# Kernel optimization log

Measured on AMD Instinct MI355X. Metric: run time of the kernel, lower is better.

## Reference

```python
import jax, jax.numpy as jnp
import numpy as np

H = 1024          # hidden_dim; also the attention 'sequence' length (embed_dim=1)
L = 12            # n_layers per stack (att1 and att2 each have L blocks)
FF = 4 * H        # MLP expansion
B, CT_DIM, CL_DIM = 8, 2048, 128
EPS = 1e-5


def _ln(x, g, b):
    m = jnp.mean(x, axis=-1, keepdims=True)
    v = jnp.mean((x - m) ** 2, axis=-1, keepdims=True)
    return (x - m) / jnp.sqrt(v + EPS) * g + b


def setup_inputs() -> dict:
    key = jax.random.key(0)
    ks = jax.random.split(key, 8)

    def w(k, shape, s=0.02):
        return (jax.random.normal(k, shape) * s).astype(jnp.float32)

    inp = {
        "ct": jax.random.normal(ks[0], (B, CT_DIM), jnp.float32),
        "clinical": jax.random.normal(ks[1], (B, CL_DIM), jnp.float32),
        "W_ct": w(ks[2], (CT_DIM, H)), "b_ct": jnp.zeros((H,), jnp.float32),
        "W_cl": w(ks[3], (CL_DIM, H)), "b_cl": jnp.zeros((H,), jnp.float32),
        "norm_g": jnp.ones((2 * H,), jnp.float32),
        "norm_b": jnp.zeros((2 * H,), jnp.float32),
    }
    for i, pre in enumerate(("att1", "att2")):
        kk = jax.random.split(ks[4 + i], 4)
        inp[pre + "_inw"] = w(kk[0], (L, 3), 0.5)      # q,k,v scalar in-proj weights (embed_dim=1)
        inp[pre + "_inb"] = jnp.zeros((L, 3), jnp.float32)
        inp[pre + "_ow"] = w(kk[1], (L,), 0.5)          # scalar out-proj weight
        inp[pre + "_ob"] = jnp.zeros((L,), jnp.float32)
        inp[pre + "_g1"] = jnp.ones((L, H), jnp.float32)
        inp[pre + "_be1"] = jnp.zeros((L, H), jnp.float32)
        inp[pre + "_g2"] = jnp.ones((L, H), jnp.float32)
        inp[pre + "_be2"] = jnp.zeros((L, H), jnp.float32)
        inp[pre + "_W1"] = w(kk[2], (L, H, FF))
        inp[pre + "_b1"] = jnp.zeros((L, FF), jnp.float32)
        inp[pre + "_W2"] = w(kk[3], (L, FF, H))
        inp[pre + "_b2"] = jnp.zeros((L, H), jnp.float32)
    return inp


def _stack(query, kv, params):
    # query is fixed across the stack; kv is the carried state (matches
    # Scale_Dot_Attention returning (query, kv, kv) through nn.Sequential).
    def step(kv, p):
        inw, inb, ow, ob, g1, be1, g2, be2, W1, b1, W2, b2 = p
        v = _ln(kv, g1, be1)                              # norm1(value)  [B,H]
        # embed_dim=1 MHA: scalar in-projections, scale = 1/sqrt(1) = 1
        qp = query * inw[0] + inb[0]                      # [B,H]
        kp = kv * inw[1] + inb[1]                         # [B,H]
        vp = v * inw[2] + inb[2]                          # [B,H]
        attn = jax.nn.softmax(qp[:, :, None] * kp[:, None, :], axis=-1)  # [B,H,H]
        av = jnp.einsum('bqk,bk->bq', attn, vp) * ow + ob                # out-proj
        out = _ln(av + v, g2, be2)                        # norm2(attn + normed value)
        out = out + jax.nn.gelu(out @ W1 + b1, approximate=False) @ W2 + b2
        return out, None
    kv, _ = jax.lax.scan(step, kv, params)
    return kv


def _forward(ct, clinical, W_ct, b_ct, W_cl, b_cl,
             att1_inw, att1_inb, att1_ow, att1_ob, att1_g1, att1_be1,
             att1_g2, att1_be2, att1_W1, att1_b1, att1_W2, att1_b2,
             att2_inw, att2_inb, att2_ow, att2_ob, att2_g1, att2_be1,
             att2_g2, att2_be2, att2_W1, att2_b1, att2_W2, att2_b2,
             norm_g, norm_b):
    cte = ct @ W_ct + b_ct            # [B,H]
    cle = clinical @ W_cl + b_cl      # [B,H]
    p1 = (att1_inw, att1_inb, att1_ow, att1_ob, att1_g1, att1_be1,
          att1_g2, att1_be2, att1_W1, att1_b1, att1_W2, att1_b2)
    p2 = (att2_inw, att2_inb, att2_ow, att2_ob, att2_g1, att2_be1,
          att2_g2, att2_be2, att2_W1, att2_b1, att2_W2, att2_b2)
    ct_attn = _stack(cle, cte, p1)    # att1: query=clinical, kv=ct
    cl_attn = _stack(cte, cle, p2)    # att2: query=ct, kv=clinical
    return _ln(jnp.concatenate([ct_attn, cl_attn], axis=1), norm_g, norm_b)


def reference(ct, clinical, W_ct, b_ct, W_cl, b_cl,
              att1_inw, att1_inb, att1_ow, att1_ob, att1_g1, att1_be1,
              att1_g2, att1_be2, att1_W1, att1_b1, att1_W2, att1_b2,
              att2_inw, att2_inb, att2_ow, att2_ob, att2_g1, att2_be1,
              att2_g2, att2_be2, att2_W1, att2_b1, att2_W2, att2_b2,
              norm_g, norm_b):
    return _forward(ct, clinical, W_ct, b_ct, W_cl, b_cl,
                    att1_inw, att1_inb, att1_ow, att1_ob, att1_g1, att1_be1,
                    att1_g2, att1_be2, att1_W1, att1_b1, att1_W2, att1_b2,
                    att2_inw, att2_inb, att2_ow, att2_ob, att2_g1, att2_be1,
                    att2_g2, att2_be2, att2_W1, att2_b1, att2_W2, att2_b2,
                    norm_g, norm_b)
```

## Files before the change

kernel.cpp:

```cpp
#include <hip/hip_runtime.h>
#include <cstddef>

namespace {

constexpr int kH = 1024;
constexpr int kFF = 4096;
constexpr int kB = 8;
constexpr int kL = 12;
constexpr float kEps = 1e-5f;

struct StackParams {
  const float *inw, *inb, *ow, *ob, *g1, *be1, *g2, *be2, *W1, *b1, *W2, *b2;
};

__device__ __forceinline__ void blkReduceSum2(float& a, float& c, float* red) {
#pragma unroll
  for (int m = 1; m < 64; m <<= 1) { a += __shfl_xor(a, m); c += __shfl_xor(c, m); }
  int w = threadIdx.x >> 6;
  __syncthreads();
  if ((threadIdx.x & 63) == 0) { red[w] = a; red[4 + w] = c; }
  __syncthreads();
  a = red[0] + red[1] + red[2] + red[3];
  c = red[4] + red[5] + red[6] + red[7];
}

__device__ __forceinline__ void blkReduceMaxMin(float& a, float& c, float* red) {
#pragma unroll
  for (int m = 1; m < 64; m <<= 1) {
    a = fmaxf(a, __shfl_xor(a, m));
    c = fminf(c, __shfl_xor(c, m));
  }
  int w = threadIdx.x >> 6;
  __syncthreads();
  if ((threadIdx.x & 63) == 0) { red[w] = a; red[4 + w] = c; }
  __syncthreads();
  a = fmaxf(fmaxf(red[0], red[1]), fmaxf(red[2], red[3]));
  c = fminf(fminf(red[4], red[5]), fminf(red[6], red[7]));
}

template <int KC>
__global__ __launch_bounds__(256) void gemvPart(const float* __restrict__ X,
                                                const float* __restrict__ W,
                                                float* __restrict__ part,
                                                int K, int N) {
  const int FT = N >> 10;
  int ft = blockIdx.x % FT;
  int kc = blockIdx.x / FT;
  int k0 = kc * KC;
  __shared__ float Xs[kB][KC];
  int t = threadIdx.x;
  for (int i = t; i < kB * KC; i += 256) {
    int b = i / KC, kk = i % KC;
    Xs[b][kk] = X[(size_t)b * K + k0 + kk];
  }
  __syncthreads();
  int c0 = (ft << 10) + (t << 2);
  float acc[kB][4];
#pragma unroll
  for (int b = 0; b < kB; ++b)
#pragma unroll
    for (int j = 0; j < 4; ++j) acc[b][j] = 0.f;
  const float* Wp = W + (size_t)k0 * N + c0;
#pragma unroll
  for (int kk = 0; kk < KC; ++kk) {
    float4 w = *reinterpret_cast<const float4*>(Wp + (size_t)kk * N);
#pragma unroll
    for (int b = 0; b < kB; ++b) {
      float x = Xs[b][kk];
      acc[b][0] = fmaf(x, w.x, acc[b][0]);
      acc[b][1] = fmaf(x, w.y, acc[b][1]);
      acc[b][2] = fmaf(x, w.z, acc[b][2]);
      acc[b][3] = fmaf(x, w.w, acc[b][3]);
    }
  }
  float* pp = part + (size_t)kc * kB * N + c0;
#pragma unroll
  for (int b = 0; b < kB; ++b) {
    *reinterpret_cast<float4*>(pp + (size_t)b * N) =
        make_float4(acc[b][0], acc[b][1], acc[b][2], acc[b][3]);
  }
}

__global__ __launch_bounds__(256) void embedReduce(const float* __restrict__ pct,
                                                   const float* __restrict__ pcl,
                                                   const float* __restrict__ b_ct,
                                                   const float* __restrict__ b_cl,
                                                   float* __restrict__ emb,
                                                   float* __restrict__ kv) {
  int id = blockIdx.x * 256 + threadIdx.x;
  int s = id >> 13;
  int bn = id & 8191;
  int n = id & 1023;
  float sum;
  if (s == 0) {
    sum = b_ct[n];
#pragma unroll 4
    for (int p = 0; p < 128; ++p) sum += pct[(size_t)p * 8192 + bn];
  } else {
    sum = b_cl[n];
#pragma unroll 4
    for (int p = 0; p < 32; ++p) sum += pcl[(size_t)p * 8192 + bn];
  }
  emb[id] = sum;
  kv[id] = sum;
}

__global__ __launch_bounds__(256) void attnKernel(const float* __restrict__ kv,
                                                  const float* __restrict__ emb,
                                                  float* __restrict__ y2,
                                                  StackParams P0, StackParams P1,
                                                  int l) {
  int bid = blockIdx.x;
  int s = bid >> 8;
  int b = (bid >> 5) & 7;
  int qt = bid & 31;
  StackParams P = s ? P1 : P0;
  const float* kvr = kv + ((size_t)((s << 3) + b)) * kH;
  const float* qr = emb + ((size_t)(((1 - s) << 3) + b)) * kH;
  float wi0 = P.inw[l * 3 + 0], wi1 = P.inw[l * 3 + 1], wi2 = P.inw[l * 3 + 2];
  float bi0 = P.inb[l * 3 + 0], bi1 = P.inb[l * 3 + 1], bi2 = P.inb[l * 3 + 2];
  float ow = P.ow[l], ob = P.ob[l];
  const float* g1 = P.g1 + (size_t)l * kH;
  const float* be1 = P.be1 + (size_t)l * kH;

  __shared__ float kvs[kH];
  __shared__ float2 kvp[kH];
  __shared__ float red[8];

  int t = threadIdx.x;
  float lsum = 0.f, lsq = 0.f;
#pragma unroll
  for (int i = 0; i < 4; ++i) {
    float x = kvr[t + 256 * i];
    kvs[t + 256 * i] = x;
    lsum += x;
    lsq += x * x;
  }
  blkReduceSum2(lsum, lsq, red);
  float mean = lsum * (1.f / kH);
  float rstd = rsqrtf(lsq * (1.f / kH) - mean * mean + kEps);

  float lmax = -1e30f, lmin = 1e30f;
#pragma unroll
  for (int i = 0; i < 4; ++i) {
    int k = t + 256 * i;
    float x = kvs[k];
    float kp = fmaf(x, wi1, bi1);
    float v = (x - mean) * rstd * g1[k] + be1[k];
    float vp = fmaf(v, wi2, bi2);
    kvp[k] = make_float2(kp, vp);
    lmax = fmaxf(lmax, kp);
    lmin = fminf(lmin, kp);
  }
  blkReduceMaxMin(lmax, lmin, red);
  __syncthreads();

  int q = (qt << 5) + (t >> 3);
  int ks = t & 7;
  float sq = fmaf(qr[q], wi0, bi0);
  float mb = fmaxf(sq * lmax, sq * lmin);
  float den0 = 0.f, num0 = 0.f, den1 = 0.f, num1 = 0.f;
#pragma unroll 4
  for (int j = 0; j < 128; j += 2) {
    float2 a = kvp[ks + (j << 3)];
    float2 c = kvp[ks + ((j + 1) << 3)];
    float e0 = __expf(fmaf(sq, a.x, -mb));
    float e1 = __expf(fmaf(sq, c.x, -mb));
    den0 += e0; num0 = fmaf(e0, a.y, num0);
    den1 += e1; num1 = fmaf(e1, c.y, num1);
  }
  float den = den0 + den1, num = num0 + num1;
#pragma unroll
  for (int m = 1; m < 8; m <<= 1) {
    den += __shfl_xor(den, m);
    num += __shfl_xor(num, m);
  }
  if (ks == 0) {
    float av = num / den;
    float vq = (kvs[q] - mean) * rstd * g1[q] + be1[q];
    y2[((size_t)((s << 3) + b)) * kH + q] = fmaf(av, ow, ob) + vq;
  }
}

__global__ __launch_bounds__(256) void gemm1Kernel(const float* __restrict__ y2,
                                                   float* __restrict__ xn,
                                                   float* __restrict__ part1,
                                                   StackParams P0, StackParams P1,
                                                   int l) {
  int bid = blockIdx.x;
  int s = bid >> 8;
  int ft = (bid >> 6) & 3;
  int kc = bid & 63;
  StackParams P = s ? P1 : P0;
  const float* y2s = y2 + ((size_t)s << 13);
  __shared__ float sm[kB], sr[kB];
  __shared__ float Xs[kB][16];
  int t = threadIdx.x;
  {
    int b = t >> 5, lane = t & 31;
    const float* row = y2s + (size_t)b * kH;
    float sum = 0.f, sq = 0.f;
    for (int i = lane; i < kH; i += 32) {
      float x = row[i];
      sum += x;
      sq += x * x;
    }
#pragma unroll
    for (int m = 1; m < 32; m <<= 1) { sum += __shfl_xor(sum, m); sq += __shfl_xor(sq, m); }
    if (lane == 0) {
      float mean = sum * (1.f / kH);
      sm[b] = mean;
      sr[b] = rsqrtf(sq * (1.f / kH) - mean * mean + kEps);
    }
  }
  __syncthreads();
  int k0 = kc << 4;
  if (t < 128) {
    int b = t >> 4, kk = t & 15, k = k0 + kk;
    float x = y2s[(size_t)b * kH + k];
    float v = (x - sm[b]) * sr[b] * P.g2[(size_t)l * kH + k] + P.be2[(size_t)l * kH + k];
    Xs[b][kk] = v;
    if (ft == 0) xn[((size_t)s << 13) + (size_t)b * kH + k] = v;
  }
  __syncthreads();
  int c0 = (ft << 10) + (t << 2);
  const float* W = P.W1 + (size_t)l * kH * kFF + (size_t)k0 * kFF + c0;
  float acc[kB][4];
#pragma unroll
  for (int b = 0; b < kB; ++b)
#pragma unroll
    for (int j = 0; j < 4; ++j) acc[b][j] = 0.f;
#pragma unroll
  for (int kk = 0; kk < 16; ++kk) {
    float4 w = *reinterpret_cast<const float4*>(W + (size_t)kk * kFF);
#pragma unroll
    for (int b = 0; b < kB; ++b) {
      float x = Xs[b][kk];
      acc[b][0] = fmaf(x, w.x, acc[b][0]);
      acc[b][1] = fmaf(x, w.y, acc[b][1]);
      acc[b][2] = fmaf(x, w.z, acc[b][2]);
      acc[b][3] = fmaf(x, w.w, acc[b][3]);
    }
  }
  float* pp = part1 + ((size_t)(s * 64 + kc) * kB) * kFF + c0;
#pragma unroll
  for (int b = 0; b < kB; ++b) {
    *reinterpret_cast<float4*>(pp + (size_t)b * kFF) =
        make_float4(acc[b][0], acc[b][1], acc[b][2], acc[b][3]);
  }
}

__global__ __launch_bounds__(256) void gemm2Kernel(const float* __restrict__ part1,
                                                   float* __restrict__ part2,
                                                   StackParams P0, StackParams P1,
                                                   int l) {
  int bid = blockIdx.x;
  int s = bid >> 8;
  int kc = bid & 255;
  StackParams P = s ? P1 : P0;
  int k0 = kc << 4;
  __shared__ float Xs[kB][16];
  int t = threadIdx.x;
  if (t < 128) {
    int b = t >> 4, kk = t & 15;
    const float* pp = part1 + (size_t)s * 64 * kB * kFF + (size_t)b * kFF + k0 + kk;
    float sum = P.b1[(size_t)l * kFF + k0 + kk];
#pragma unroll 8
    for (int p = 0; p < 64; ++p) sum += pp[(size_t)p * kB * kFF];
    Xs[b][kk] = 0.5f * sum * (1.f + erff(sum * 0.70710678118654752f));
  }
  __syncthreads();
  int c0 = t << 2;
  const float* W = P.W2 + (size_t)l * kFF * kH + (size_t)k0 * kH + c0;
  float acc[kB][4];
#pragma unroll
  for (int b = 0; b < kB; ++b)
#pragma unroll
    for (int j = 0; j < 4; ++j) acc[b][j] = 0.f;
#pragma unroll
  for (int kk = 0; kk < 16; ++kk) {
    float4 w = *reinterpret_cast<const float4*>(W + (size_t)kk * kH);
#pragma unroll
    for (int b = 0; b < kB; ++b) {
      float x = Xs[b][kk];
      acc[b][0] = fmaf(x, w.x, acc[b][0]);
      acc[b][1] = fmaf(x, w.y, acc[b][1]);
      acc[b][2] = fmaf(x, w.z, acc[b][2]);
      acc[b][3] = fmaf(x, w.w, acc[b][3]);
    }
  }
  float* pp = part2 + ((size_t)(s * 256 + kc) * kB) * kH + c0;
#pragma unroll
  for (int b = 0; b < kB; ++b) {
    *reinterpret_cast<float4*>(pp + (size_t)b * kH) =
        make_float4(acc[b][0], acc[b][1], acc[b][2], acc[b][3]);
  }
}

__global__ __launch_bounds__(256) void reduce2Kernel(const float* __restrict__ part2,
                                                     const float* __restrict__ xn,
                                                     float* __restrict__ kv,
                                                     StackParams P0, StackParams P1,
                                                     int l) {
  int gid = blockIdx.x * 256 + threadIdx.x;
  int o = gid >> 2;
  int ks = gid & 3;
  int s = o >> 13;
  int bn = o & 8191;
  int n = o & 1023;
  const float* pp = part2 + (size_t)s * 256 * 8192 + (size_t)ks * 8192 + bn;
  float sum = 0.f;
#pragma unroll 8
  for (int j = 0; j < 64; ++j) sum += pp[(size_t)j * 4 * 8192];
  sum += __shfl_xor(sum, 1);
  sum += __shfl_xor(sum, 2);
  if (ks == 0) {
    StackParams P = s ? P1 : P0;
    kv[o] = sum + P.b2[(size_t)l * kH + n] + xn[o];
  }
}

__global__ __launch_bounds__(256) void finalLn(const float* __restrict__ kv,
                                               const float* __restrict__ g,
                                               const float* __restrict__ bb,
                                               float* __restrict__ out) {
  int b = blockIdx.x;
  int t = threadIdx.x;
  __shared__ float red[8];
  float vals[8];
  float sum = 0.f, sq = 0.f;
#pragma unroll
  for (int i = 0; i < 8; ++i) {
    int idx = t + 256 * i;
    int s = idx >> 10, n = idx & 1023;
    float x = kv[(size_t)s * 8192 + (size_t)b * kH + n];
    vals[i] = x;
    sum += x;
    sq += x * x;
  }
  blkReduceSum2(sum, sq, red);
  float mean = sum * (1.f / 2048.f);
  float rstd = rsqrtf(sq * (1.f / 2048.f) - mean * mean + kEps);
#pragma unroll
  for (int i = 0; i < 8; ++i) {
    int idx = t + 256 * i;
    out[(size_t)b * 2048 + idx] = (vals[i] - mean) * rstd * g[idx] + bb[idx];
  }
}

}

extern "C" void kernel_launch(void* const* d_in, const int* in_sizes, int n_in,
                              void* d_out, int out_size, void* d_ws, size_t ws_size,
                              hipStream_t stream) {
  const float* ct = (const float*)d_in[0];
  const float* clinical = (const float*)d_in[1];
  const float* W_ct = (const float*)d_in[2];
  const float* b_ct = (const float*)d_in[3];
  const float* W_cl = (const float*)d_in[4];
  const float* b_cl = (const float*)d_in[5];
  const float* norm_g = (const float*)d_in[6];
  const float* norm_b = (const float*)d_in[7];

  StackParams P0{(const float*)d_in[8],  (const float*)d_in[9],  (const float*)d_in[10],
                 (const float*)d_in[11], (const float*)d_in[12], (const float*)d_in[13],
                 (const float*)d_in[14], (const float*)d_in[15], (const float*)d_in[16],
                 (const float*)d_in[17], (const float*)d_in[18], (const float*)d_in[19]};
  StackParams P1{(const float*)d_in[20], (const float*)d_in[21], (const float*)d_in[22],
                 (const float*)d_in[23], (const float*)d_in[24], (const float*)d_in[25],
                 (const float*)d_in[26], (const float*)d_in[27], (const float*)d_in[28],
                 (const float*)d_in[29], (const float*)d_in[30], (const float*)d_in[31]};

  float* ws = (float*)d_ws;
  float* emb = ws;
  float* kv = emb + 2 * kB * kH;
  float* y2 = kv + 2 * kB * kH;
  float* xn = y2 + 2 * kB * kH;
  float* part1 = xn + 2 * kB * kH;
  float* part2 = part1 + (size_t)2 * 64 * kB * kFF;
  float* pct = part1;
  float* pcl = part1 + (size_t)128 * kB * kH;

  gemvPart<16><<<128, 256, 0, stream>>>(ct, W_ct, pct, 2048, 1024);
  gemvPart<4><<<32, 256, 0, stream>>>(clinical, W_cl, pcl, 128, 1024);
  embedReduce<<<64, 256, 0, stream>>>(pct, pcl, b_ct, b_cl, emb, kv);

  for (int l = 0; l < kL; ++l) {
    attnKernel<<<512, 256, 0, stream>>>(kv, emb, y2, P0, P1, l);
    gemm1Kernel<<<512, 256, 0, stream>>>(y2, xn, part1, P0, P1, l);
    gemm2Kernel<<<512, 256, 0, stream>>>(part1, part2, P0, P1, l);
    reduce2Kernel<<<256, 256, 0, stream>>>(part2, xn, kv, P0, P1, l);
  }

  finalLn<<<8, 256, 0, stream>>>(kv, norm_g, norm_b, (float*)d_out);
}
```

Measured before the change: 627.8 us.

## Fuse whole forward into one persistent cooperative kernel with grid syncs

```diff
diff --git a/kernel.cpp b/kernel.cpp
--- a/kernel.cpp
+++ b/kernel.cpp
@@ -1,5 +1,8 @@
 #include <hip/hip_runtime.h>
+#include <hip/hip_cooperative_groups.h>
 #include <cstddef>
+
+namespace cg = cooperative_groups;
 
 namespace {
 
@@ -8,23 +11,33 @@
 constexpr int kB = 8;
 constexpr int kL = 12;
 constexpr float kEps = 1e-5f;
+constexpr int NBLK = 256;
+constexpr int NTHR = 512;
 
 struct StackParams {
   const float *inw, *inb, *ow, *ob, *g1, *be1, *g2, *be2, *W1, *b1, *W2, *b2;
 };
 
-__device__ __forceinline__ void blkReduceSum2(float& a, float& c, float* red) {
+struct KArgs {
+  float *emb, *kv0, *y2, *xn, *part1, *part2, *pct, *pcl;
+  const float *ct, *clinical, *W_ct, *b_ct, *W_cl, *b_cl, *norm_g, *norm_b;
+  StackParams P0, P1;
+  float* out;
+};
+
+__device__ __forceinline__ void blkRed2(float& a, float& c, float* red) {
 #pragma unroll
   for (int m = 1; m < 64; m <<= 1) { a += __shfl_xor(a, m); c += __shfl_xor(c, m); }
   int w = threadIdx.x >> 6;
   __syncthreads();
-  if ((threadIdx.x & 63) == 0) { red[w] = a; red[4 + w] = c; }
-  __syncthreads();
-  a = red[0] + red[1] + red[2] + red[3];
-  c = red[4] + red[5] + red[6] + red[7];
-}
-
-__device__ __forceinline__ void blkReduceMaxMin(float& a, float& c, float* red) {
+  if ((threadIdx.x & 63) == 0) { red[w] = a; red[8 + w] = c; }
+  __syncthreads();
+  a = 0.f; c = 0.f;
+#pragma unroll
+  for (int j = 0; j < 8; ++j) { a += red[j]; c += red[8 + j]; }
+}
+
+__device__ __forceinline__ void blkRedMaxMin(float& a, float& c, float* red) {
 #pragma unroll
   for (int m = 1; m < 64; m <<= 1) {
     a = fmaxf(a, __shfl_xor(a, m));
@@ -32,319 +45,278 @@
   }
   int w = threadIdx.x >> 6;
   __syncthreads();
-  if ((threadIdx.x & 63) == 0) { red[w] = a; red[4 + w] = c; }
-  __syncthreads();
-  a = fmaxf(fmaxf(red[0], red[1]), fmaxf(red[2], red[3]));
-  c = fminf(fminf(red[4], red[5]), fminf(red[6], red[7]));
-}
-
-template <int KC>
-__global__ __launch_bounds__(256) void gemvPart(const float* __restrict__ X,
-                                                const float* __restrict__ W,
-                                                float* __restrict__ part,
-                                                int K, int N) {
-  const int FT = N >> 10;
-  int ft = blockIdx.x % FT;
-  int kc = blockIdx.x / FT;
-  int k0 = kc * KC;
-  __shared__ float Xs[kB][KC];
-  int t = threadIdx.x;
-  for (int i = t; i < kB * KC; i += 256) {
-    int b = i / KC, kk = i % KC;
-    Xs[b][kk] = X[(size_t)b * K + k0 + kk];
-  }
-  __syncthreads();
-  int c0 = (ft << 10) + (t << 2);
+  if ((threadIdx.x & 63) == 0) { red[w] = a; red[8 + w] = c; }
+  __syncthreads();
+  float ra = red[0], rc = red[8];
+#pragma unroll
+  for (int j = 1; j < 8; ++j) { ra = fmaxf(ra, red[j]); rc = fminf(rc, red[8 + j]); }
+  a = ra; c = rc;
+}
+
+__device__ __forceinline__ void reduce8store(float acc[kB][4], float* s_red,
+                                             float* dst, int N, int c0, int t) {
+  int w = t >> 6, lane = t & 63;
+  float* slot = s_red + (size_t)((w & 3) * 64 + lane) * 33;
+  if (w >= 4) {
+#pragma unroll
+    for (int f = 0; f < 32; ++f) slot[f] = acc[f >> 2][f & 3];
+  }
+  __syncthreads();
+  if (w < 4) {
+#pragma unroll
+    for (int f = 0; f < 32; ++f) slot[f] += acc[f >> 2][f & 3];
+  }
+  __syncthreads();
+  if (t < 256) {
+    int lane2 = t & 63, p = t >> 6;
+#pragma unroll
+    for (int bb = 0; bb < 2; ++bb) {
+      int b = p * 2 + bb, f0 = b * 4;
+      float4 s = make_float4(0.f, 0.f, 0.f, 0.f);
+#pragma unroll
+      for (int ww = 0; ww < 4; ++ww) {
+        const float* q = s_red + (size_t)(ww * 64 + lane2) * 33 + f0;
+        s.x += q[0]; s.y += q[1]; s.z += q[2]; s.w += q[3];
+      }
+      *reinterpret_cast<float4*>(dst + (size_t)b * N + c0 + lane2 * 4) = s;
+    }
+  }
+  __syncthreads();
+}
+
+template <int RPW, int ROWS>
+__device__ __forceinline__ void gemvTile(const float* __restrict__ Wrow, int N,
+                                         const float* Xs, float* dstSlice,
+                                         int c0, float* s_red, int t) {
+  int w = t >> 6, lane = t & 63;
   float acc[kB][4];
 #pragma unroll
-  for (int b = 0; b < kB; ++b)
-#pragma unroll
-    for (int j = 0; j < 4; ++j) acc[b][j] = 0.f;
-  const float* Wp = W + (size_t)k0 * N + c0;
-#pragma unroll
-  for (int kk = 0; kk < KC; ++kk) {
-    float4 w = *reinterpret_cast<const float4*>(Wp + (size_t)kk * N);
+  for (int b = 0; b < kB; ++b) { acc[b][0] = acc[b][1] = acc[b][2] = acc[b][3] = 0.f; }
+  const float* Wp = Wrow + (size_t)(w * RPW) * N + c0 + (lane << 2);
+#pragma unroll
+  for (int i = 0; i < RPW; ++i) {
+    float4 wv = *reinterpret_cast<const float4*>(Wp + (size_t)i * N);
+    int r = w * RPW + i;
 #pragma unroll
     for (int b = 0; b < kB; ++b) {
-      float x = Xs[b][kk];
-      acc[b][0] = fmaf(x, w.x, acc[b][0]);
-      acc[b][1] = fmaf(x, w.y, acc[b][1]);
-      acc[b][2] = fmaf(x, w.z, acc[b][2]);
-      acc[b][3] = fmaf(x, w.w, acc[b][3]);
-    }
-  }
-  float* pp = part + (size_t)kc * kB * N + c0;
-#pragma unroll
-  for (int b = 0; b < kB; ++b) {
-    *reinterpret_cast<float4*>(pp + (size_t)b * N) =
-        make_float4(acc[b][0], acc[b][1], acc[b][2], acc[b][3]);
-  }
-}
-
-__global__ __launch_bounds__(256) void embedReduce(const float* __restrict__ pct,
-                                                   const float* __restrict__ pcl,
-                                                   const float* __restrict__ b_ct,
-                                                   const float* __restrict__ b_cl,
-                                                   float* __restrict__ emb,
-                                                   float* __restrict__ kv) {
-  int id = blockIdx.x * 256 + threadIdx.x;
-  int s = id >> 13;
-  int bn = id & 8191;
-  int n = id & 1023;
-  float sum;
-  if (s == 0) {
-    sum = b_ct[n];
+      float x = Xs[b * ROWS + r];
+      acc[b][0] = fmaf(x, wv.x, acc[b][0]);
+      acc[b][1] = fmaf(x, wv.y, acc[b][1]);
+      acc[b][2] = fmaf(x, wv.z, acc[b][2]);
+      acc[b][3] = fmaf(x, wv.w, acc[b][3]);
+    }
+  }
+  reduce8store(acc, s_red, dstSlice, N, c0, t);
+}
+
+__global__ __launch_bounds__(NTHR, 2) void fusedAll(KArgs a) {
+  cg::grid_group grid = cg::this_grid();
+  __shared__ float s_xs[1024];
+  __shared__ float s_red[4 * 64 * 33];
+  __shared__ float s_stats[32];
+
+  const int bid = blockIdx.x;
+  const int t = threadIdx.x;
+
+  if (bid < 128) {
+    int kc = bid >> 2, fc = bid & 3;
+    int k0 = kc * 64, c0 = fc * 256;
+    { int b = t >> 6, r = t & 63; s_xs[b * 64 + r] = a.ct[b * 2048 + k0 + r]; }
+    __syncthreads();
+    gemvTile<8, 64>(a.W_ct + (size_t)k0 * kH, kH, s_xs,
+                    a.pct + (size_t)kc * kB * kH, c0, s_red, t);
+  } else if (bid < 160) {
+    int bb = bid - 128;
+    int kc = bb >> 2, fc = bb & 3;
+    int k0 = kc * 16, c0 = fc * 256;
+    if (t < 128) { int b = t >> 4, r = t & 15; s_xs[b * 16 + r] = a.clinical[b * 128 + k0 + r]; }
+    __syncthreads();
+    gemvTile<2, 16>(a.W_cl + (size_t)k0 * kH, kH, s_xs,
+                    a.pcl + (size_t)kc * kB * kH, c0, s_red, t);
+  }
+  grid.sync();
+
+  if (bid < 32) {
+    int id = bid * NTHR + t;
+    int s = id >> 13, n = id & 1023, bn = id & 8191;
+    float sum;
+    if (s == 0) {
+      sum = a.b_ct[n];
+      const float* pp = a.pct + bn;
 #pragma unroll 4
-    for (int p = 0; p < 128; ++p) sum += pct[(size_t)p * 8192 + bn];
-  } else {
-    sum = b_cl[n];
+      for (int p = 0; p < 32; ++p) sum += pp[(size_t)p * 8192];
+    } else {
+      sum = a.b_cl[n];
+      const float* pp = a.pcl + bn;
+#pragma unroll
+      for (int p = 0; p < 8; ++p) sum += pp[(size_t)p * 8192];
+    }
+    a.emb[id] = sum;
+    a.kv0[id] = sum;
+  }
+  grid.sync();
+
+  for (int l = 0; l < kL; ++l) {
+    {
+      int s = bid >> 7, b = (bid >> 4) & 7, qt = bid & 15;
+      const StackParams& P = s ? a.P1 : a.P0;
+      const float* qr = a.emb + (size_t)((1 - s) * 8 + b) * kH;
+      float wi0 = P.inw[l * 3 + 0], wi1 = P.inw[l * 3 + 1], wi2 = P.inw[l * 3 + 2];
+      float bi0 = P.inb[l * 3 + 0], bi1 = P.inb[l * 3 + 1], bi2 = P.inb[l * 3 + 2];
+      float ow = P.ow[l], ob = P.ob[l];
+      const float* g1 = P.g1 + (size_t)l * kH;
+      const float* be1 = P.be1 + (size_t)l * kH;
+      float2* kvp = reinterpret_cast<float2*>(s_red);
+
+      float lsum = 0.f, lsq = 0.f;
+#pragma unroll
+      for (int i = 0; i < 2; ++i) {
+        int n = t + i * NTHR;
+        float x;
+        if (l == 0) {
+          x = a.kv0[(size_t)(s * 8 + b) * kH + n];
+        } else {
+          x = P.b2[(size_t)(l - 1) * kH + n] + a.xn[(size_t)(s * 8 + b) * kH + n];
+          const float* pp = a.part2 + ((size_t)(s * 32) * kB + b) * kH + n;
+#pragma unroll 8
+          for (int p = 0; p < 32; ++p) x += pp[(size_t)p * kB * kH];
+        }
+        s_xs[n] = x;
+        lsum += x;
+        lsq += x * x;
+      }
+      blkRed2(lsum, lsq, s_stats);
+      float mean = lsum * (1.f / kH);
+      float rstd = rsqrtf(lsq * (1.f / kH) - mean * mean + kEps);
+
+      float lmax = -1e30f, lmin = 1e30f;
+#pragma unroll
+      for (int i = 0; i < 2; ++i) {
+        int n = t + i * NTHR;
+        float x = s_xs[n];
+        float kp = fmaf(x, wi1, bi1);
+        float v = (x - mean) * rstd * g1[n] + be1[n];
+        float vp = fmaf(v, wi2, bi2);
+        kvp[n] = make_float2(kp, vp);
+        lmax = fmaxf(lmax, kp);
+        lmin = fminf(lmin, kp);
+      }
+      blkRedMaxMin(lmax, lmin, s_stats);
+
+      int q = qt * 64 + (t >> 3), ks = t & 7;
+      float sq_ = fmaf(qr[q], wi0, bi0);
+      float mb = fmaxf(sq_ * lmax, sq_ * lmin);
+      float den0 = 0.f, num0 = 0.f, den1 = 0.f, num1 = 0.f;
 #pragma unroll 4
-    for (int p = 0; p < 32; ++p) sum += pcl[(size_t)p * 8192 + bn];
-  }
-  emb[id] = sum;
-  kv[id] = sum;
-}
-
-__global__ __launch_bounds__(256) void attnKernel(const float* __restrict__ kv,
-                                                  const float* __restrict__ emb,
-                                                  float* __restrict__ y2,
-                                                  StackParams P0, StackParams P1,
-                                                  int l) {
-  int bid = blockIdx.x;
-  int s = bid >> 8;
-  int b = (bid >> 5) & 7;
-  int qt = bid & 31;
-  StackParams P = s ? P1 : P0;
-  const float* kvr = kv + ((size_t)((s << 3) + b)) * kH;
-  const float* qr = emb + ((size_t)(((1 - s) << 3) + b)) * kH;
-  float wi0 = P.inw[l * 3 + 0], wi1 = P.inw[l * 3 + 1], wi2 = P.inw[l * 3 + 2];
-  float bi0 = P.inb[l * 3 + 0], bi1 = P.inb[l * 3 + 1], bi2 = P.inb[l * 3 + 2];
-  float ow = P.ow[l], ob = P.ob[l];
-  const float* g1 = P.g1 + (size_t)l * kH;
-  const float* be1 = P.be1 + (size_t)l * kH;
-
-  __shared__ float kvs[kH];
-  __shared__ float2 kvp[kH];
-  __shared__ float red[8];
-
-  int t = threadIdx.x;
-  float lsum = 0.f, lsq = 0.f;
-#pragma unroll
-  for (int i = 0; i < 4; ++i) {
-    float x = kvr[t + 256 * i];
-    kvs[t + 256 * i] = x;
-    lsum += x;
-    lsq += x * x;
-  }
-  blkReduceSum2(lsum, lsq, red);
-  float mean = lsum * (1.f / kH);
-  float rstd = rsqrtf(lsq * (1.f / kH) - mean * mean + kEps);
-
-  float lmax = -1e30f, lmin = 1e30f;
-#pragma unroll
-  for (int i = 0; i < 4; ++i) {
-    int k = t + 256 * i;
-    float x = kvs[k];
-    float kp = fmaf(x, wi1, bi1);
-    float v = (x - mean) * rstd * g1[k] + be1[k];
-    float vp = fmaf(v, wi2, bi2);
-    kvp[k] = make_float2(kp, vp);
-    lmax = fmaxf(lmax, kp);
-    lmin = fminf(lmin, kp);
-  }
-  blkReduceMaxMin(lmax, lmin, red);
-  __syncthreads();
-
-  int q = (qt << 5) + (t >> 3);
-  int ks = t & 7;
-  float sq = fmaf(qr[q], wi0, bi0);
-  float mb = fmaxf(sq * lmax, sq * lmin);
-  float den0 = 0.f, num0 = 0.f, den1 = 0.f, num1 = 0.f;
+      for (int j = 0; j < 128; j += 2) {
+        float2 av = kvp[ks + (j << 3)];
+        float2 cv = kvp[ks + ((j + 1) << 3)];
+        float e0 = __expf(fmaf(sq_, av.x, -mb));
+        float e1 = __expf(fmaf(sq_, cv.x, -mb));
+        den0 += e0; num0 = fmaf(e0, av.y, num0);
+        den1 += e1; num1 = fmaf(e1, cv.y, num1);
+      }
+      float den = den0 + den1, num = num0 + num1;
+#pragma unroll
+      for (int m = 1; m < 8; m <<= 1) {
+        den += __shfl_xor(den, m);
+        num += __shfl_xor(num, m);
+      }
+      if (ks == 0) {
+        float av = num / den;
+        float vq = (s_xs[q] - mean) * rstd * g1[q] + be1[q];
+        a.y2[(size_t)(s * 8 + b) * kH + q] = fmaf(av, ow, ob) + vq;
+      }
+    }
+    grid.sync();
+
+    {
+      int s = bid >> 7, kc = (bid >> 4) & 7, fc = bid & 15;
+      const StackParams& P = s ? a.P1 : a.P0;
+      int k0 = kc * 128, c0 = fc * 256;
+      const float* y2s = a.y2 + (size_t)s * 8192;
+      {
+        int w = t >> 6, lane = t & 63;
+        float sum = 0.f, sq = 0.f;
+#pragma unroll
+        for (int j = 0; j < 16; ++j) {
+          float x = y2s[w * 1024 + lane + 64 * j];
+          sum += x;
+          sq += x * x;
+        }
+#pragma unroll
+        for (int m = 1; m < 64; m <<= 1) { sum += __shfl_xor(sum, m); sq += __shfl_xor(sq, m); }
+        if (lane == 0) {
+          float mean = sum * (1.f / kH);
+          s_stats[w] = mean;
+          s_stats[8 + w] = rsqrtf(sq * (1.f / kH) - mean * mean + kEps);
+        }
+      }
+      __syncthreads();
+      const float* g2p = P.g2 + (size_t)l * kH + k0;
+      const float* be2p = P.be2 + (size_t)l * kH + k0;
+#pragma unroll
+      for (int i = 0; i < 2; ++i) {
+        int idx = t + i * NTHR;
+        int b = idx >> 7, r = idx & 127;
+        float x = y2s[b * 1024 + k0 + r];
+        float v = (x - s_stats[b]) * s_stats[8 + b] * g2p[r] + be2p[r];
+        s_xs[b * 128 + r] = v;
+        if (fc == 0) a.xn[(size_t)(s * 8 + b) * kH + k0 + r] = v;
+      }
+      __syncthreads();
+      gemvTile<16, 128>(P.W1 + (size_t)l * kH * kFF + (size_t)k0 * kFF, kFF,
+                        s_xs, a.part1 + (size_t)(s * 8 + kc) * kB * kFF, c0, s_red, t);
+    }
+    grid.sync();
+
+    {
+      int s = bid >> 7, kc = (bid >> 2) & 31, fc = bid & 3;
+      const StackParams& P = s ? a.P1 : a.P0;
+      int k0 = kc * 128, c0 = fc * 256;
+      const float* b1p = P.b1 + (size_t)l * kFF + k0;
+#pragma unroll
+      for (int i = 0; i < 2; ++i) {
+        int idx = t + i * NTHR;
+        int b = idx >> 7, r = idx & 127;
+        const float* pp = a.part1 + ((size_t)(s * 8) * kB + b) * kFF + k0 + r;
+        float h = b1p[r];
+#pragma unroll
+        for (int p = 0; p < 8; ++p) h += pp[(size_t)p * kB * kFF];
+        s_xs[b * 128 + r] = 0.5f * h * (1.f + erff(h * 0.70710678118654752f));
+      }
+      __syncthreads();
+      gemvTile<16, 128>(P.W2 + (size_t)l * kFF * kH + (size_t)k0 * kH, kH,
+                        s_xs, a.part2 + (size_t)(s * 32 + kc) * kB * kH, c0, s_red, t);
+    }
+    grid.sync();
+  }
+
+  if (bid < 8) {
+    int b = bid;
+    float vals[4];
+    float lsum = 0.f, lsq = 0.f;
+#pragma unroll
+    for (int i = 0; i < 4; ++i) {
+      int idx = t + i * NTHR;
+      int s = idx >> 10, n = idx & 1023;
+      const StackParams& P = s ? a.P1 : a.P0;
+      float x = P.b2[(size_t)(kL - 1) * kH + n] + a.xn[(size_t)(s * 8 + b) * kH + n];
+      const float* pp = a.part2 + ((size_t)(s * 32) * kB + b) * kH + n;
 #pragma unroll 4
-  for (int j = 0; j < 128; j += 2) {
-    float2 a = kvp[ks + (j << 3)];
-    float2 c = kvp[ks + ((j + 1) << 3)];
-    float e0 = __expf(fmaf(sq, a.x, -mb));
-    float e1 = __expf(fmaf(sq, c.x, -mb));
-    den0 += e0; num0 = fmaf(e0, a.y, num0);
-    den1 += e1; num1 = fmaf(e1, c.y, num1);
-  }
-  float den = den0 + den1, num = num0 + num1;
-#pragma unroll
-  for (int m = 1; m < 8; m <<= 1) {
-    den += __shfl_xor(den, m);
-    num += __shfl_xor(num, m);
-  }
-  if (ks == 0) {
-    float av = num / den;
-    float vq = (kvs[q] - mean) * rstd * g1[q] + be1[q];
-    y2[((size_t)((s << 3) + b)) * kH + q] = fmaf(av, ow, ob) + vq;
-  }
-}
-
-__global__ __launch_bounds__(256) void gemm1Kernel(const float* __restrict__ y2,
-                                                   float* __restrict__ xn,
-                                                   float* __restrict__ part1,
-                                                   StackParams P0, StackParams P1,
-                                                   int l) {
-  int bid = blockIdx.x;
-  int s = bid >> 8;
-  int ft = (bid >> 6) & 3;
-  int kc = bid & 63;
-  StackParams P = s ? P1 : P0;
-  const float* y2s = y2 + ((size_t)s << 13);
-  __shared__ float sm[kB], sr[kB];
-  __shared__ float Xs[kB][16];
-  int t = threadIdx.x;
-  {
-    int b = t >> 5, lane = t & 31;
-    const float* row = y2s + (size_t)b * kH;
-    float sum = 0.f, sq = 0.f;
-    for (int i = lane; i < kH; i += 32) {
-      float x = row[i];
-      sum += x;
-      sq += x * x;
-    }
-#pragma unroll
-    for (int m = 1; m < 32; m <<= 1) { sum += __shfl_xor(sum, m); sq += __shfl_xor(sq, m); }
-    if (lane == 0) {
-      float mean = sum * (1.f / kH);
-      sm[b] = mean;
-      sr[b] = rsqrtf(sq * (1.f / kH) - mean * mean + kEps);
-    }
-  }
-  __syncthreads();
-  int k0 = kc << 4;
-  if (t < 128) {
-    int b = t >> 4, kk = t & 15, k = k0 + kk;
-    float x = y2s[(size_t)b * kH + k];
-    float v = (x - sm[b]) * sr[b] * P.g2[(size_t)l * kH + k] + P.be2[(size_t)l * kH + k];
-    Xs[b][kk] = v;
-    if (ft == 0) xn[((size_t)s << 13) + (size_t)b * kH + k] = v;
-  }
-  __syncthreads();
-  int c0 = (ft << 10) + (t << 2);
-  const float* W = P.W1 + (size_t)l * kH * kFF + (size_t)k0 * kFF + c0;
-  float acc[kB][4];
-#pragma unroll
-  for (int b = 0; b < kB; ++b)
-#pragma unroll
-    for (int j = 0; j < 4; ++j) acc[b][j] = 0.f;
-#pragma unroll
-  for (int kk = 0; kk < 16; ++kk) {
-    float4 w = *reinterpret_cast<const float4*>(W + (size_t)kk * kFF);
-#pragma unroll
-    for (int b = 0; b < kB; ++b) {
-      float x = Xs[b][kk];
-      acc[b][0] = fmaf(x, w.x, acc[b][0]);
-      acc[b][1] = fmaf(x, w.y, acc[b][1]);
-      acc[b][2] = fmaf(x, w.z, acc[b][2]);
-      acc[b][3] = fmaf(x, w.w, acc[b][3]);
-    }
-  }
-  float* pp = part1 + ((size_t)(s * 64 + kc) * kB) * kFF + c0;
-#pragma unroll
-  for (int b = 0; b < kB; ++b) {
-    *reinterpret_cast<float4*>(pp + (size_t)b * kFF) =
-        make_float4(acc[b][0], acc[b][1], acc[b][2], acc[b][3]);
-  }
-}
-
-__global__ __launch_bounds__(256) void gemm2Kernel(const float* __restrict__ part1,
-                                                   float* __restrict__ part2,
-                                                   StackParams P0, StackParams P1,
-                                                   int l) {
-  int bid = blockIdx.x;
-  int s = bid >> 8;
-  int kc = bid & 255;
-  StackParams P = s ? P1 : P0;
-  int k0 = kc << 4;
-  __shared__ float Xs[kB][16];
-  int t = threadIdx.x;
-  if (t < 128) {
-    int b = t >> 4, kk = t & 15;
-    const float* pp = part1 + (size_t)s * 64 * kB * kFF + (size_t)b * kFF + k0 + kk;
-    float sum = P.b1[(size_t)l * kFF + k0 + kk];
-#pragma unroll 8
-    for (int p = 0; p < 64; ++p) sum += pp[(size_t)p * kB * kFF];
-    Xs[b][kk] = 0.5f * sum * (1.f + erff(sum * 0.70710678118654752f));
-  }
-  __syncthreads();
-  int c0 = t << 2;
-  const float* W = P.W2 + (size_t)l * kFF * kH + (size_t)k0 * kH + c0;
-  float acc[kB][4];
-#pragma unroll
-  for (int b = 0; b < kB; ++b)
-#pragma unroll
-    for (int j = 0; j < 4; ++j) acc[b][j] = 0.f;
-#pragma unroll
-  for (int kk = 0; kk < 16; ++kk) {
-    float4 w = *reinterpret_cast<const float4*>(W + (size_t)kk * kH);
-#pragma unroll
-    for (int b = 0; b < kB; ++b) {
-      float x = Xs[b][kk];
-      acc[b][0] = fmaf(x, w.x, acc[b][0]);
-      acc[b][1] = fmaf(x, w.y, acc[b][1]);
-      acc[b][2] = fmaf(x, w.z, acc[b][2]);
-      acc[b][3] = fmaf(x, w.w, acc[b][3]);
-    }
-  }
-  float* pp = part2 + ((size_t)(s * 256 + kc) * kB) * kH + c0;
-#pragma unroll
-  for (int b = 0; b < kB; ++b) {
-    *reinterpret_cast<float4*>(pp + (size_t)b * kH) =
-        make_float4(acc[b][0], acc[b][1], acc[b][2], acc[b][3]);
-  }
-}
-
-__global__ __launch_bounds__(256) void reduce2Kernel(const float* __restrict__ part2,
-                                                     const float* __restrict__ xn,
-                                                     float* __restrict__ kv,
-                                                     StackParams P0, StackParams P1,
-                                                     int l) {
-  int gid = blockIdx.x * 256 + threadIdx.x;
-  int o = gid >> 2;
-  int ks = gid & 3;
-  int s = o >> 13;
-  int bn = o & 8191;
-  int n = o & 1023;
-  const float* pp = part2 + (size_t)s * 256 * 8192 + (size_t)ks * 8192 + bn;
-  float sum = 0.f;
-#pragma unroll 8
-  for (int j = 0; j < 64; ++j) sum += pp[(size_t)j * 4 * 8192];
-  sum += __shfl_xor(sum, 1);
-  sum += __shfl_xor(sum, 2);
-  if (ks == 0) {
-    StackParams P = s ? P1 : P0;
-    kv[o] = sum + P.b2[(size_t)l * kH + n] + xn[o];
-  }
-}
-
-__global__ __launch_bounds__(256) void finalLn(const float* __restrict__ kv,
-                                               const float* __restrict__ g,
-                                               const float* __restrict__ bb,
-                                               float* __restrict__ out) {
-  int b = blockIdx.x;
-  int t = threadIdx.x;
-  __shared__ float red[8];
-  float vals[8];
-  float sum = 0.f, sq = 0.f;
-#pragma unroll
-  for (int i = 0; i < 8; ++i) {
-    int idx = t + 256 * i;
-    int s = idx >> 10, n = idx & 1023;
-    float x = kv[(size_t)s * 8192 + (size_t)b * kH + n];
-    vals[i] = x;
-    sum += x;
-    sq += x * x;
-  }
-  blkReduceSum2(sum, sq, red);
-  float mean = sum * (1.f / 2048.f);
-  float rstd = rsqrtf(sq * (1.f / 2048.f) - mean * mean + kEps);
-#pragma unroll
-  for (int i = 0; i < 8; ++i) {
-    int idx = t + 256 * i;
-    out[(size_t)b * 2048 + idx] = (vals[i] - mean) * rstd * g[idx] + bb[idx];
+      for (int p = 0; p < 32; ++p) x += pp[(size_t)p * kB * kH];
+      vals[i] = x;
+      lsum += x;
+      lsq += x * x;
+    }
+    blkRed2(lsum, lsq, s_stats);
+    float mean = lsum * (1.f / 2048.f);
+    float rstd = rsqrtf(lsq * (1.f / 2048.f) - mean * mean + kEps);
+#pragma unroll
+    for (int i = 0; i < 4; ++i) {
+      int idx = t + i * NTHR;
+      a.out[(size_t)b * 2048 + idx] = (vals[i] - mean) * rstd * a.norm_g[idx] + a.norm_b[idx];
+    }
   }
 }
 
@@ -353,44 +325,36 @@
 extern "C" void kernel_launch(void* const* d_in, const int* in_sizes, int n_in,
                               void* d_out, int out_size, void* d_ws, size_t ws_size,
                               hipStream_t stream) {
-  const float* ct = (const float*)d_in[0];
-  const float* clinical = (const float*)d_in[1];
-  const float* W_ct = (const float*)d_in[2];
-  const float* b_ct = (const float*)d_in[3];
-  const float* W_cl = (const float*)d_in[4];
-  const float* b_cl = (const float*)d_in[5];
-  const float* norm_g = (const float*)d_in[6];
-  const float* norm_b = (const float*)d_in[7];
-
-  StackParams P0{(const float*)d_in[8],  (const float*)d_in[9],  (const float*)d_in[10],
-                 (const float*)d_in[11], (const float*)d_in[12], (const float*)d_in[13],
-                 (const float*)d_in[14], (const float*)d_in[15], (const float*)d_in[16],
-                 (const float*)d_in[17], (const float*)d_in[18], (const float*)d_in[19]};
-  StackParams P1{(const float*)d_in[20], (const float*)d_in[21], (const float*)d_in[22],
-                 (const float*)d_in[23], (const float*)d_in[24], (const float*)d_in[25],
-                 (const float*)d_in[26], (const float*)d_in[27], (const float*)d_in[28],
-                 (const float*)d_in[29], (const float*)d_in[30], (const float*)d_in[31]};
-
-  float* ws = (float*)d_ws;
-  float* emb = ws;
-  float* kv = emb + 2 * kB * kH;
-  float* y2 = kv + 2 * kB * kH;
-  float* xn = y2 + 2 * kB * kH;
-  float* part1 = xn + 2 * kB * kH;
-  float* part2 = part1 + (size_t)2 * 64 * kB * kFF;
-  float* pct = part1;
-  float* pcl = part1 + (size_t)128 * kB * kH;
-
-  gemvPart<16><<<128, 256, 0, stream>>>(ct, W_ct, pct, 2048, 1024);
-  gemvPart<4><<<32, 256, 0, stream>>>(clinical, W_cl, pcl, 128, 1024);
-  embedReduce<<<64, 256, 0, stream>>>(pct, pcl, b_ct, b_cl, emb, kv);
-
-  for (int l = 0; l < kL; ++l) {
-    attnKernel<<<512, 256, 0, stream>>>(kv, emb, y2, P0, P1, l);
-    gemm1Kernel<<<512, 256, 0, stream>>>(y2, xn, part1, P0, P1, l);
-    gemm2Kernel<<<512, 256, 0, stream>>>(part1, part2, P0, P1, l);
-    reduce2Kernel<<<256, 256, 0, stream>>>(part2, xn, kv, P0, P1, l);
-  }
-
-  finalLn<<<8, 256, 0, stream>>>(kv, norm_g, norm_b, (float*)d_out);
-}
+  KArgs ka;
+  ka.ct = (const float*)d_in[0];
+  ka.clinical = (const float*)d_in[1];
+  ka.W_ct = (const float*)d_in[2];
+  ka.b_ct = (const float*)d_in[3];
+  ka.W_cl = (const float*)d_in[4];
+  ka.b_cl = (const float*)d_in[5];
+  ka.norm_g = (const float*)d_in[6];
+  ka.norm_b = (const float*)d_in[7];
+
+  ka.P0 = StackParams{(const float*)d_in[8],  (const float*)d_in[9],  (const float*)d_in[10],
+                      (const float*)d_in[11], (const float*)d_in[12], (const float*)d_in[13],
+                      (const float*)d_in[14], (const float*)d_in[15], (const float*)d_in[16],
+                      (const float*)d_in[17], (const float*)d_in[18], (const float*)d_in[19]};
+  ka.P1 = StackParams{(const float*)d_in[20], (const float*)d_in[21], (const float*)d_in[22],
+                      (const float*)d_in[23], (const float*)d_in[24], (const float*)d_in[25],
+                      (const float*)d_in[26], (const float*)d_in[27], (const float*)d_in[28],
+                      (const float*)d_in[29], (const float*)d_in[30], (const float*)d_in[31]};
+
+  float* base = (float*)d_ws;
+  ka.emb = base;
+  ka.kv0 = ka.emb + 2 * kB * kH;
+  ka.y2 = ka.kv0 + 2 * kB * kH;
+  ka.xn = ka.y2 + 2 * kB * kH;
+  ka.part1 = ka.xn + 2 * kB * kH;
+  ka.part2 = ka.part1 + (size_t)2 * 8 * kB * kFF;
+  ka.pct = ka.part2 + (size_t)2 * 32 * kB * kH;
+  ka.pcl = ka.pct + (size_t)32 * kB * kH;
+  ka.out = (float*)d_out;
+
+  void* params[] = {&ka};
+  hipLaunchCooperativeKernel((void*)fusedAll, dim3(NBLK), dim3(NTHR), params, 0, stream);
+}
```

After: 1.539 ms. 2.45x slower.
